# Kernel optimization log

Measured on AMD Instinct MI355X. Metric: run time of the kernel, lower is better.

The kernel has to match this reference:

```python
import jax, jax.numpy as jnp
import numpy as np
import math

DIM = 256
N = 4096
E = 1024
NEG = -1.0e9


def setup_inputs() -> dict:
    key = jax.random.key(0)
    ks = jax.random.split(key, 10)
    x = jax.random.normal(ks[0], (N, DIM), dtype=jnp.float32)
    # sparse incidence / adjacency (module only uses >0 as mask)
    H = (jax.random.uniform(ks[1], (N, E)) < 0.05).astype(jnp.float32)
    adj = (jax.random.uniform(ks[2], (N, N)) < 0.01).astype(jnp.float32)
    s = 1.0 / math.sqrt(DIM)
    W_he = jax.random.normal(ks[3], (DIM, DIM), dtype=jnp.float32) * s  # HyperedgeAttention.W
    u = jax.random.normal(ks[4], (DIM,), dtype=jnp.float32)            # HyperedgeAttention.u
    W_e = jax.random.normal(ks[5], (DIM, DIM), dtype=jnp.float32) * s  # NodeAttention.W_e
    W_n = jax.random.normal(ks[6], (DIM, DIM), dtype=jnp.float32) * s  # NodeAttention.W_n
    W_g = jax.random.normal(ks[7], (DIM, DIM), dtype=jnp.float32) * s  # GraphAttention.W
    a_g = jax.random.normal(ks[8], (2 * DIM,), dtype=jnp.float32) * s  # GraphAttention.attn weight
    return {"x": x, "H": H, "adj": adj, "W_he": W_he, "u": u,
            "W_e": W_e, "W_n": W_n, "W_g": W_g, "a_g": a_g}


def reference(x, H, adj, W_he, u, W_e, W_n, W_g, a_g):
    n, dim = x.shape
    inv_sqrt_d = 1.0 / math.sqrt(dim)
    maskH = H > 0                       # [N,E] bool
    mask_Hf = maskH.astype(x.dtype)

    # ---- HyperedgeAttention ----
    h_he = x @ W_he                     # [N,dim]
    sc = (h_he @ u) * inv_sqrt_d        # [N]
    scE = jnp.where(maskH, sc[:, None], NEG)      # [N,E]
    A = jax.nn.softmax(scE, axis=0) * mask_Hf     # column softmax over nodes
    e_repr = A.T @ h_he                 # [E,dim]

    # ---- NodeAttention (only B is used) ----
    hn = x @ W_n                        # [N,dim]
    he = e_repr @ W_e                   # [E,dim]
    Bsc = jnp.where(maskH, (hn @ he.T) * inv_sqrt_d, NEG)
    B = jax.nn.softmax(Bsc, axis=1) * mask_Hf     # [N,E]

    # ---- GraphAttention (concat score split: e_ij = lrelu(h_i.a1 + h_j.a2)) ----
    h_g = x @ W_g                       # [N,dim]
    s1 = h_g @ a_g[:dim]                # [N]
    s2 = h_g @ a_g[dim:]                # [N]
    e = jax.nn.leaky_relu(s1[:, None] + s2[None, :], 0.2)   # [N,N]
    maskA = (adj > 0).astype(x.dtype)
    sl = jnp.eye(n, dtype=x.dtype)
    e = e * (maskA + sl) - 1e9 * jnp.clip(1.0 - maskA - sl, 0.0, None)
    G = jax.nn.softmax(e, axis=1)       # [N,N]

    # ---- Mixing ----
    he_sz = jnp.clip(mask_Hf.sum(0), 1.0, None)   # [E]
    M = (G @ mask_Hf) / he_sz[None, :]            # [N,E]
    A_hat = jax.nn.softmax(A.T + M.T, axis=1) * mask_Hf.T   # [E,N]
    e_mix = A_hat @ (x @ W_he)                    # [E,dim]
    B_hat = jax.nn.softmax(B + M, axis=1) * mask_Hf          # [N,E]
    z_h = jax.nn.elu(B_hat @ (e_mix @ W_e))       # [N,dim]
    G_hat = jax.nn.softmax(G + B @ B.T + A @ A.T, axis=1)    # [N,N]
    z_g = jax.nn.elu(G_hat @ (x @ W_g))           # [N,dim]
    return z_h, z_g
```

## Files before the change

### kernel.cpp

```cpp
#include <hip/hip_runtime.h>
#include <math.h>
#include <stdint.h>

#define Nn 4096
#define Ee 1024
#define Dd 256

typedef __attribute__((ext_vector_type(8))) __bf16 bf16x8;
typedef __attribute__((ext_vector_type(4))) float f32x4;
typedef __attribute__((ext_vector_type(8))) unsigned short u16x8;

__device__ __forceinline__ unsigned short f2bf(float f) {
  unsigned int u = __float_as_uint(f);
  unsigned int r = (u + 0x7fffu + ((u >> 16) & 1u)) >> 16;
  return (unsigned short)r;
}

__device__ __forceinline__ void gload_lds16(const void* g, void* l) {
  __builtin_amdgcn_global_load_lds(
      (__attribute__((address_space(1))) void*)const_cast<void*>(g),
      (__attribute__((address_space(3))) void*)l, 16, 0, 0);
}

__device__ __forceinline__ float block_reduce_sum(float v) {
  __shared__ float sh[4];
  #pragma unroll
  for (int o = 32; o > 0; o >>= 1) v += __shfl_down(v, o);
  int lane = threadIdx.x & 63, w = threadIdx.x >> 6;
  if (lane == 0) sh[w] = v;
  __syncthreads();
  float s = sh[0] + sh[1] + sh[2] + sh[3];
  __syncthreads();
  return s;
}

__global__ __launch_bounds__(256) void gemm_bt_bf16(
    const unsigned short* __restrict__ Ab, const unsigned short* __restrict__ Bb,
    float* __restrict__ Cp, int M, int N, int K, const float* __restrict__ coldiv)
{
  __shared__ unsigned short As[2][128 * 32];
  __shared__ unsigned short Bs[2][128 * 32];
  const int tid = threadIdx.x;
  const int m0 = blockIdx.x * 128, n0 = blockIdx.y * 128;
  const int wave = tid >> 6, lane = tid & 63;
  const int wr = (wave >> 1) * 64, wc = (wave & 1) * 64;
  const int l16 = lane & 15, lq = lane >> 4;
  f32x4 acc[4][4] = {};
  const int NT = K >> 5;

  auto stage = [&](int buf, int kt) {
    const int k0 = kt * 32;
    #pragma unroll
    for (int i = 0; i < 2; ++i) {
      int t2 = tid + i * 256;
      int r = t2 >> 2, c = (t2 & 3) * 8;
      gload_lds16(Ab + (size_t)(m0 + r) * K + k0 + c, &As[buf][t2 * 8]);
    }
    #pragma unroll
    for (int i = 0; i < 2; ++i) {
      int t2 = tid + i * 256;
      int r = t2 >> 2, c = (t2 & 3) * 8;
      gload_lds16(Bb + (size_t)(n0 + r) * K + k0 + c, &Bs[buf][t2 * 8]);
    }
  };

  stage(0, 0);
  __syncthreads();
  int buf = 0;
  for (int kt = 0; kt < NT; ++kt) {
    if (kt + 1 < NT) stage(buf ^ 1, kt + 1);
    bf16x8 af[4], bfr[4];
    #pragma unroll
    for (int m = 0; m < 4; ++m)
      af[m] = *reinterpret_cast<const bf16x8*>(&As[buf][(wr + m * 16 + l16) * 32 + lq * 8]);
    #pragma unroll
    for (int n = 0; n < 4; ++n)
      bfr[n] = *reinterpret_cast<const bf16x8*>(&Bs[buf][(wc + n * 16 + l16) * 32 + lq * 8]);
    #pragma unroll
    for (int m = 0; m < 4; ++m)
      #pragma unroll
      for (int n = 0; n < 4; ++n)
        acc[m][n] = __builtin_amdgcn_mfma_f32_16x16x32_bf16(af[m], bfr[n], acc[m][n], 0, 0, 0);
    __syncthreads();
    buf ^= 1;
  }
  #pragma unroll
  for (int m = 0; m < 4; ++m)
    #pragma unroll
    for (int n = 0; n < 4; ++n) {
      int col = n0 + wc + n * 16 + l16;
      float cd = coldiv ? fmaxf(coldiv[col], 1.f) : 1.f;
      #pragma unroll
      for (int q = 0; q < 4; ++q) {
        int row = m0 + wr + m * 16 + lq * 4 + q;
        Cp[(size_t)row * N + col] = acc[m][n][q] / cd;
      }
    }
}

__global__ __launch_bounds__(256) void gemm_gram_k(
    const unsigned short* __restrict__ CAT,
    float* __restrict__ G,
    float* __restrict__ rowsum)
{
  const int K = 2048, N = Nn;
  __shared__ unsigned short As[2][128 * 32];
  __shared__ unsigned short Bs[2][128 * 32];
  const int tid = threadIdx.x;
  const int m0 = blockIdx.x * 128, n0 = blockIdx.y * 128;
  const int wave = tid >> 6, lane = tid & 63;
  const int wr = (wave >> 1) * 64, wc = (wave & 1) * 64;
  const int l16 = lane & 15, lq = lane >> 4;
  f32x4 acc[4][4] = {};
  const int NT = K >> 5;

  auto stage = [&](int buf, int kt) {
    const int k0 = kt * 32;
    #pragma unroll
    for (int i = 0; i < 2; ++i) {
      int t2 = tid + i * 256;
      int r = t2 >> 2, c = (t2 & 3) * 8;
      gload_lds16(CAT + (size_t)(m0 + r) * K + k0 + c, &As[buf][t2 * 8]);
    }
    #pragma unroll
    for (int i = 0; i < 2; ++i) {
      int t2 = tid + i * 256;
      int r = t2 >> 2, c = (t2 & 3) * 8;
      gload_lds16(CAT + (size_t)(n0 + r) * K + k0 + c, &Bs[buf][t2 * 8]);
    }
  };

  stage(0, 0);
  __syncthreads();
  int buf = 0;
  for (int kt = 0; kt < NT; ++kt) {
    if (kt + 1 < NT) stage(buf ^ 1, kt + 1);
    bf16x8 af[4], bfr[4];
    #pragma unroll
    for (int m = 0; m < 4; ++m)
      af[m] = *reinterpret_cast<const bf16x8*>(&As[buf][(wr + m * 16 + l16) * 32 + lq * 8]);
    #pragma unroll
    for (int n = 0; n < 4; ++n)
      bfr[n] = *reinterpret_cast<const bf16x8*>(&Bs[buf][(wc + n * 16 + l16) * 32 + lq * 8]);
    #pragma unroll
    for (int m = 0; m < 4; ++m)
      #pragma unroll
      for (int n = 0; n < 4; ++n)
        acc[m][n] = __builtin_amdgcn_mfma_f32_16x16x32_bf16(af[m], bfr[n], acc[m][n], 0, 0, 0);
    __syncthreads();
    buf ^= 1;
  }
  #pragma unroll
  for (int m = 0; m < 4; ++m)
    #pragma unroll
    for (int q = 0; q < 4; ++q) {
      int row = m0 + wr + m * 16 + lq * 4 + q;
      float s = 0.f;
      #pragma unroll
      for (int n = 0; n < 4; ++n) {
        int col = n0 + wc + n * 16 + l16;
        size_t idx = (size_t)row * N + col;
        float e = expf(G[idx] + acc[m][n][q]);
        G[idx] = e;
        s += e;
      }
      s += __shfl_xor(s, 1); s += __shfl_xor(s, 2);
      s += __shfl_xor(s, 4); s += __shfl_xor(s, 8);
      if (l16 == 0) atomicAdd(&rowsum[row], s);
    }
}

__global__ __launch_bounds__(256) void gemm64s_bt_bf16(
    const unsigned short* __restrict__ Ab, const unsigned short* __restrict__ Bb,
    float* __restrict__ Cp, int M, int N, int K, int KS)
{
  __shared__ unsigned short As[2][64 * 64];
  __shared__ unsigned short Bs[2][64 * 64];
  const int tid = threadIdx.x;
  const int m0 = blockIdx.x * 64, n0 = blockIdx.y * 64;
  const int kbase = blockIdx.z * KS;
  const int wave = tid >> 6, lane = tid & 63;
  const int wr = (wave >> 1) * 32, wc = (wave & 1) * 32;
  const int l16 = lane & 15, lq = lane >> 4;
  f32x4 acc[2][2] = {};
  const int NT = KS >> 6;

  auto stage = [&](int buf, int kt) {
    const int k0 = kbase + kt * 64;
    #pragma unroll
    for (int i = 0; i < 2; ++i) {
      int t2 = tid + i * 256;
      int r = t2 >> 3, c = (t2 & 7) * 8;
      gload_lds16(Ab + (size_t)(m0 + r) * K + k0 + c, &As[buf][t2 * 8]);
    }
    #pragma unroll
    for (int i = 0; i < 2; ++i) {
      int t2 = tid + i * 256;
      int r = t2 >> 3, c = (t2 & 7) * 8;
      gload_lds16(Bb + (size_t)(n0 + r) * K + k0 + c, &Bs[buf][t2 * 8]);
    }
  };

  stage(0, 0);
  __syncthreads();
  int buf = 0;
  for (int kt = 0; kt < NT; ++kt) {
    if (kt + 1 < NT) stage(buf ^ 1, kt + 1);
    bf16x8 af[2][2], bfr[2][2];
    #pragma unroll
    for (int m = 0; m < 2; ++m)
      #pragma unroll
      for (int ks = 0; ks < 2; ++ks)
        af[m][ks] = *reinterpret_cast<const bf16x8*>(
            &As[buf][(wr + m * 16 + l16) * 64 + ks * 32 + lq * 8]);
    #pragma unroll
    for (int n = 0; n < 2; ++n)
      #pragma unroll
      for (int ks = 0; ks < 2; ++ks)
        bfr[n][ks] = *reinterpret_cast<const bf16x8*>(
            &Bs[buf][(wc + n * 16 + l16) * 64 + ks * 32 + lq * 8]);
    #pragma unroll
    for (int m = 0; m < 2; ++m)
      #pragma unroll
      for (int n = 0; n < 2; ++n)
        #pragma unroll
        for (int ks = 0; ks < 2; ++ks)
          acc[m][n] = __builtin_amdgcn_mfma_f32_16x16x32_bf16(af[m][ks], bfr[n][ks], acc[m][n], 0, 0, 0);
    __syncthreads();
    buf ^= 1;
  }
  #pragma unroll
  for (int m = 0; m < 2; ++m)
    #pragma unroll
    for (int n = 0; n < 2; ++n) {
      int col = n0 + wc + n * 16 + l16;
      #pragma unroll
      for (int q = 0; q < 4; ++q) {
        int row = m0 + wr + m * 16 + lq * 4 + q;
        atomicAdd(&Cp[(size_t)row * N + col], acc[m][n][q]);
      }
    }
}

__global__ __launch_bounds__(256) void tcvt_k(const float* __restrict__ in,
                                              unsigned short* __restrict__ outT, int R, int S) {
  __shared__ unsigned short tile[64][65];
  int r0 = blockIdx.x * 64, c0 = blockIdx.y * 64;
  int t = threadIdx.x & 63, q = threadIdx.x >> 6;
  for (int rr = q; rr < 64; rr += 4)
    tile[t][rr] = f2bf(in[(long)(r0 + rr) * S + c0 + t]);
  __syncthreads();
  for (int cc = q; cc < 64; cc += 4)
    outT[(long)(c0 + cc) * R + r0 + t] = tile[cc][t];
}

__global__ __launch_bounds__(256) void elu_k(float* __restrict__ p, long n) {
  long i = ((long)blockIdx.x * 256 + threadIdx.x) * 4;
  if (i + 4 > n) return;
  float4 v = *reinterpret_cast<const float4*>(&p[i]);
  v.x = v.x > 0.f ? v.x : expm1f(v.x);
  v.y = v.y > 0.f ? v.y : expm1f(v.y);
  v.z = v.z > 0.f ? v.z : expm1f(v.z);
  v.w = v.w > 0.f ? v.w : expm1f(v.w);
  *reinterpret_cast<float4*>(&p[i]) = v;
}

__global__ __launch_bounds__(256) void wcat_k(const float* __restrict__ W0,
                                              const float* __restrict__ W1,
                                              const float* __restrict__ W2,
                                              float* __restrict__ Wcat) {
  int k = blockIdx.x, s = blockIdx.y, t = threadIdx.x;
  const float* W = s == 0 ? W0 : (s == 1 ? W1 : W2);
  Wcat[(long)k * 768 + s * 256 + t] = W[(long)k * 256 + t];
}

__global__ __launch_bounds__(256) void gemm64_k(
    const float* __restrict__ Ap, const float* __restrict__ Bp, float* __restrict__ Cp,
    int M, int N, int K, int Asm, int Ask, int Bsk, int Bsn)
{
  __shared__ alignas(16) float As[16][68];
  __shared__ alignas(16) float Bs[16][68];
  const int tid = threadIdx.x;
  const int tx = tid & 15, ty = tid >> 4;
  const int m0 = blockIdx.x * 64, n0 = blockIdx.y * 64;
  float acc[4][4] = {};
  for (int k0 = 0; k0 < K; k0 += 16) {
    if (Ask == 1) {
      int mm = tid >> 2, kk = (tid & 3) << 2;
      float4 v = *reinterpret_cast<const float4*>(&Ap[(long)(m0 + mm) * Asm + k0 + kk]);
      As[kk + 0][mm] = v.x; As[kk + 1][mm] = v.y; As[kk + 2][mm] = v.z; As[kk + 3][mm] = v.w;
    } else {
      int kk = tid >> 4, mm = (tid & 15) << 2;
      *reinterpret_cast<float4*>(&As[kk][mm]) =
          *reinterpret_cast<const float4*>(&Ap[(long)(k0 + kk) * Ask + m0 + mm]);
    }
    if (Bsn == 1) {
      int kk = tid >> 4, nn = (tid & 15) << 2;
      *reinterpret_cast<float4*>(&Bs[kk][nn]) =
          *reinterpret_cast<const float4*>(&Bp[(long)(k0 + kk) * Bsk + n0 + nn]);
    } else {
      int nn = tid >> 2, kk = (tid & 3) << 2;
      float4 v = *reinterpret_cast<const float4*>(&Bp[(long)(n0 + nn) * Bsn + k0 + kk]);
      Bs[kk + 0][nn] = v.x; Bs[kk + 1][nn] = v.y; Bs[kk + 2][nn] = v.z; Bs[kk + 3][nn] = v.w;
    }
    __syncthreads();
    #pragma unroll
    for (int kk = 0; kk < 16; ++kk) {
      float4 av = *reinterpret_cast<const float4*>(&As[kk][ty << 2]);
      float4 bv = *reinterpret_cast<const float4*>(&Bs[kk][tx << 2]);
      float a[4] = {av.x, av.y, av.z, av.w};
      float b[4] = {bv.x, bv.y, bv.z, bv.w};
      #pragma unroll
      for (int r = 0; r < 4; ++r)
        #pragma unroll
        for (int c = 0; c < 4; ++c) acc[r][c] = fmaf(a[r], b[c], acc[r][c]);
    }
    __syncthreads();
  }
  #pragma unroll
  for (int r = 0; r < 4; ++r) {
    long base = (long)(m0 + (ty << 2) + r) * N + n0 + (tx << 2);
    float4 o = {acc[r][0], acc[r][1], acc[r][2], acc[r][3]};
    *reinterpret_cast<float4*>(&Cp[base]) = o;
  }
}

__global__ __launch_bounds__(256) void gemm128_k(
    const float* __restrict__ Ap, const float* __restrict__ Bp, float* __restrict__ Cp,
    int M, int N, int K, int Asm, int Bsn, float alpha)
{
  __shared__ alignas(16) float As[16][132];
  __shared__ alignas(16) float Bs[16][132];
  const int tid = threadIdx.x;
  const int tx = tid & 15, ty = tid >> 4;
  const int m0 = blockIdx.x * 128, n0 = blockIdx.y * 128;
  float acc[2][2][4][4] = {};
  for (int k0 = 0; k0 < K; k0 += 16) {
    {
      int mm = tid >> 2, kk = (tid & 3) << 2;
      #pragma unroll
      for (int h = 0; h < 2; ++h) {
        float4 v = *reinterpret_cast<const float4*>(&Ap[(long)(m0 + mm + 64 * h) * Asm + k0 + kk]);
        As[kk + 0][mm + 64 * h] = v.x; As[kk + 1][mm + 64 * h] = v.y;
        As[kk + 2][mm + 64 * h] = v.z; As[kk + 3][mm + 64 * h] = v.w;
      }
    }
    {
      int nn = tid >> 2, kk = (tid & 3) << 2;
      #pragma unroll
      for (int h = 0; h < 2; ++h) {
        float4 v = *reinterpret_cast<const float4*>(&Bp[(long)(n0 + nn + 64 * h) * Bsn + k0 + kk]);
        Bs[kk + 0][nn + 64 * h] = v.x; Bs[kk + 1][nn + 64 * h] = v.y;
        Bs[kk + 2][nn + 64 * h] = v.z; Bs[kk + 3][nn + 64 * h] = v.w;
      }
    }
    __syncthreads();
    #pragma unroll
    for (int kk = 0; kk < 16; ++kk) {
      float a[2][4], b[2][4];
      #pragma unroll
      for (int h = 0; h < 2; ++h) {
        float4 av = *reinterpret_cast<const float4*>(&As[kk][(ty << 2) + 64 * h]);
        a[h][0] = av.x; a[h][1] = av.y; a[h][2] = av.z; a[h][3] = av.w;
        float4 bv = *reinterpret_cast<const float4*>(&Bs[kk][(tx << 2) + 64 * h]);
        b[h][0] = bv.x; b[h][1] = bv.y; b[h][2] = bv.z; b[h][3] = bv.w;
      }
      #pragma unroll
      for (int i = 0; i < 2; ++i)
        #pragma unroll
        for (int j = 0; j < 2; ++j)
          #pragma unroll
          for (int r = 0; r < 4; ++r)
            #pragma unroll
            for (int c = 0; c < 4; ++c)
              acc[i][j][r][c] = fmaf(a[i][r], b[j][c], acc[i][j][r][c]);
    }
    __syncthreads();
  }
  #pragma unroll
  for (int i = 0; i < 2; ++i)
    #pragma unroll
    for (int r = 0; r < 4; ++r) {
      int row = m0 + 64 * i + (ty << 2) + r;
      #pragma unroll
      for (int j = 0; j < 2; ++j) {
        long base = (long)row * N + n0 + 64 * j + (tx << 2);
        float4 o = {acc[i][j][r][0] * alpha, acc[i][j][r][1] * alpha,
                    acc[i][j][r][2] * alpha, acc[i][j][r][3] * alpha};
        *reinterpret_cast<float4*>(&Cp[base]) = o;
      }
    }
}

__global__ __launch_bounds__(256) void rowdots_k(
    const float* __restrict__ hcat, const float* __restrict__ u, const float* __restrict__ a_g,
    float* __restrict__ esc, float* __restrict__ s1, float* __restrict__ s2)
{
  int i = blockIdx.x, t = threadIdx.x;
  float hh = hcat[(long)i * 768 + t];
  float hg = hcat[(long)i * 768 + 512 + t];
  float d0 = block_reduce_sum(hh * u[t]);
  float d1 = block_reduce_sum(hg * a_g[t]);
  float d2 = block_reduce_sum(hg * a_g[Dd + t]);
  if (t == 0) {
    esc[i] = expf(d0 * 0.0625f);
    s1[i] = d1;
    s2[i] = d2;
  }
}

__global__ __launch_bounds__(256) void colstats_k(
    const float* __restrict__ H, const float* __restrict__ esc,
    float* __restrict__ colden, float* __restrict__ cnt)
{
  int e = blockIdx.x * 256 + threadIdx.x;
  int r0 = blockIdx.y * 128;
  float d = 0.f, c = 0.f;
  for (int r = r0; r < r0 + 128; ++r) {
    float h = H[(long)r * Ee + e];
    if (h > 0.f) { d += esc[r]; c += 1.f; }
  }
  atomicAdd(&colden[e], d);
  atomicAdd(&cnt[e], c);
}

__global__ __launch_bounds__(256) void fillA_k(
    const float* __restrict__ H, const float* __restrict__ esc,
    const float* __restrict__ colden, float* __restrict__ A,
    unsigned short* __restrict__ CAT)
{
  long base = ((long)blockIdx.x * 256 + threadIdx.x) * 4;
  int r = (int)(base >> 10);
  int e = (int)(base & 1023);
  float4 h = *reinterpret_cast<const float4*>(&H[base]);
  float4 cd = *reinterpret_cast<const float4*>(&colden[e]);
  float er = esc[r];
  float4 o;
  o.x = h.x > 0.f ? er / cd.x : 0.f;
  o.y = h.y > 0.f ? er / cd.y : 0.f;
  o.z = h.z > 0.f ? er / cd.z : 0.f;
  o.w = h.w > 0.f ? er / cd.w : 0.f;
  *reinterpret_cast<float4*>(&A[base]) = o;
  ushort4 ob = {f2bf(o.x), f2bf(o.y), f2bf(o.z), f2bf(o.w)};
  *reinterpret_cast<ushort4*>(&CAT[(long)r * 2048 + 1024 + e]) = ob;
}

__global__ __launch_bounds__(256) void brow_k(float* __restrict__ Bbuf,
                                              const float* __restrict__ H,
                                              unsigned short* __restrict__ CAT)
{
  int i = blockIdx.x, t = threadIdx.x;
  long base = (long)i * Ee + t * 4;
  float4 raw = *reinterpret_cast<const float4*>(&Bbuf[base]);
  float4 h = *reinterpret_cast<const float4*>(&H[base]);
  float rr[4] = {raw.x, raw.y, raw.z, raw.w}, hh[4] = {h.x, h.y, h.z, h.w};
  float p[4]; float s = 0.f;
  #pragma unroll
  for (int k = 0; k < 4; ++k) { p[k] = hh[k] > 0.f ? expf(rr[k]) : 0.f; s += p[k]; }
  float den = block_reduce_sum(s);
  float inv = den > 0.f ? 1.f / den : 0.f;
  float4 o = {p[0] * inv, p[1] * inv, p[2] * inv, p[3] * inv};
  *reinterpret_cast<float4*>(&Bbuf[base]) = o;
  ushort4 ob = {f2bf(o.x), f2bf(o.y), f2bf(o.z), f2bf(o.w)};
  *reinterpret_cast<ushort4*>(&CAT[(long)i * 2048 + t * 4]) = ob;
}

__global__ __launch_bounds__(256) void gfill_k(
    const float* __restrict__ adj, const float* __restrict__ s1,
    const float* __restrict__ s2, float* __restrict__ G, unsigned short* __restrict__ Gb)
{
  int i = blockIdx.x, t = threadIdx.x;
  float s1i = s1[i];
  float p[16]; float sum = 0.f;
  #pragma unroll
  for (int c = 0; c < 4; ++c) {
    int j = c * 1024 + t * 4;
    float4 a = *reinterpret_cast<const float4*>(&adj[(long)i * Nn + j]);
    float4 sv = *reinterpret_cast<const float4*>(&s2[j]);
    float aa[4] = {a.x, a.y, a.z, a.w}, ss[4] = {sv.x, sv.y, sv.z, sv.w};
    #pragma unroll
    for (int k = 0; k < 4; ++k) {
      float f = (aa[k] > 0.f ? 1.f : 0.f) + ((j + k) == i ? 1.f : 0.f);
      float l = s1i + ss[k];
      l = l > 0.f ? l : 0.2f * l;
      float val = l * f - 1e9f * fmaxf(1.f - f, 0.f);
      float pp = expf(val);
      p[c * 4 + k] = pp; sum += pp;
    }
  }
  float den = block_reduce_sum(sum);
  float inv = 1.f / den;
  #pragma unroll
  for (int c = 0; c < 4; ++c) {
    int j = c * 1024 + t * 4;
    float4 o = {p[c * 4] * inv, p[c * 4 + 1] * inv, p[c * 4 + 2] * inv, p[c * 4 + 3] * inv};
    *reinterpret_cast<float4*>(&G[(long)i * Nn + j]) = o;
    ushort4 ob = {f2bf(o.x), f2bf(o.y), f2bf(o.z), f2bf(o.w)};
    *reinterpret_cast<ushort4*>(&Gb[(long)i * Nn + j]) = ob;
  }
}

__global__ __launch_bounds__(256) void gscale_k(const float* __restrict__ expG,
                                                const float* __restrict__ rowsum,
                                                unsigned short* __restrict__ Gb)
{
  long i = ((long)blockIdx.x * 256 + threadIdx.x) * 8;
  int row = (int)(i >> 12);
  float inv = 1.f / rowsum[row];
  float4 a = *reinterpret_cast<const float4*>(&expG[i]);
  float4 b = *reinterpret_cast<const float4*>(&expG[i + 4]);
  u16x8 o;
  o[0] = f2bf(a.x * inv); o[1] = f2bf(a.y * inv); o[2] = f2bf(a.z * inv); o[3] = f2bf(a.w * inv);
  o[4] = f2bf(b.x * inv); o[5] = f2bf(b.y * inv); o[6] = f2bf(b.z * inv); o[7] = f2bf(b.w * inv);
  *reinterpret_cast<u16x8*>(&Gb[i]) = o;
}

__global__ __launch_bounds__(256) void amstats_k(
    const float* __restrict__ A, const float* __restrict__ Mm, float* __restrict__ aden)
{
  int e = blockIdx.x * 256 + threadIdx.x;
  int r0 = blockIdx.y * 128;
  float d = 0.f;
  for (int r = r0; r < r0 + 128; ++r) {
    long idx = (long)r * Ee + e;
    d += expf(A[idx] + Mm[idx]);
  }
  atomicAdd(&aden[e], d);
}

__global__ __launch_bounds__(256) void ahat_k(
    const float* __restrict__ Abuf, const float* __restrict__ Mm,
    const float* __restrict__ H, const float* __restrict__ aden,
    unsigned short* __restrict__ AhB)
{
  __shared__ float tile[64][65];
  int j0 = blockIdx.x * 64, e0 = blockIdx.y * 64;
  int te = threadIdx.x & 63;
  int tq = threadIdx.x >> 6;
  int e = e0 + te;
  float inv = 1.f / aden[e];
  for (int jj = tq; jj < 64; jj += 4) {
    long idx = (long)(j0 + jj) * Ee + e;
    float val = (H[idx] > 0.f) ? expf(Abuf[idx] + Mm[idx]) * inv : 0.f;
    tile[te][jj] = val;
  }
  __syncthreads();
  for (int ee = tq; ee < 64; ee += 4)
    AhB[(long)(e0 + ee) * Nn + j0 + te] = f2bf(tile[ee][te]);
}

__global__ __launch_bounds__(256) void bhat_k(const float* __restrict__ Bbuf,
                                              const float* __restrict__ Mm,
                                              const float* __restrict__ H,
                                              unsigned short* __restrict__ Bb2)
{
  int i = blockIdx.x, t = threadIdx.x;
  long base = (long)i * Ee + t * 4;
  float4 b = *reinterpret_cast<const float4*>(&Bbuf[base]);
  float4 m = *reinterpret_cast<const float4*>(&Mm[base]);
  float4 h = *reinterpret_cast<const float4*>(&H[base]);
  float bb[4] = {b.x, b.y, b.z, b.w}, mm2[4] = {m.x, m.y, m.z, m.w}, hh[4] = {h.x, h.y, h.z, h.w};
  float p[4]; float s = 0.f;
  #pragma unroll
  for (int k = 0; k < 4; ++k) { p[k] = expf(bb[k] + mm2[k]); s += p[k]; }
  float den = block_reduce_sum(s);
  float inv = 1.f / den;
  #pragma unroll
  for (int k = 0; k < 4; ++k) p[k] = hh[k] > 0.f ? p[k] * inv : 0.f;
  ushort4 ob = {f2bf(p[0]), f2bf(p[1]), f2bf(p[2]), f2bf(p[3])};
  *reinterpret_cast<ushort4*>(&Bb2[base]) = ob;
}

extern "C" void kernel_launch(void* const* d_in, const int* in_sizes, int n_in,
                              void* d_out, int out_size, void* d_ws, size_t ws_size,
                              hipStream_t stream) {
  const float* x    = (const float*)d_in[0];
  const float* H    = (const float*)d_in[1];
  const float* adj  = (const float*)d_in[2];
  const float* W_he = (const float*)d_in[3];
  const float* u    = (const float*)d_in[4];
  const float* W_e  = (const float*)d_in[5];
  const float* W_n  = (const float*)d_in[6];
  const float* W_g  = (const float*)d_in[7];
  const float* a_g  = (const float*)d_in[8];
  float* out = (float*)d_out;
  float* ws  = (float*)d_ws;
  (void)in_sizes; (void)n_in; (void)out_size; (void)ws_size;

  size_t off = 0;
  auto alloc = [&](size_t n) { float* p = ws + off; off += n; return p; };
  float* hcat   = alloc((size_t)Nn * 768);
  float* Wcat   = alloc((size_t)Dd * 768);
  float* esc    = alloc(Nn);
  float* s1     = alloc(Nn);
  float* s2     = alloc(Nn);
  float* colden = alloc(Ee);
  float* cnt    = alloc(Ee);
  float* aden   = alloc(Ee);
  float* rowsum = alloc(Nn);
  float* e_repr = alloc((size_t)Ee * Dd);
  float* e_mix  = alloc((size_t)Ee * Dd);
  float* heb    = alloc((size_t)Ee * Dd);
  float* tmp_ew = alloc((size_t)Ee * Dd);
  float* Abuf   = alloc((size_t)Nn * Ee);
  float* Bbuf   = alloc((size_t)Nn * Ee);
  float* Mm     = alloc((size_t)Nn * Ee);
  float* G      = alloc((size_t)Nn * Nn);
  unsigned short* Gb   = (unsigned short*)alloc((size_t)Nn * Nn / 2);
  unsigned short* CAT  = (unsigned short*)alloc((size_t)Nn * 2048 / 2);
  unsigned short* Hbt  = (unsigned short*)alloc((size_t)Ee * Nn / 2);
  unsigned short* AbT  = (unsigned short*)alloc((size_t)Ee * Nn / 2);
  unsigned short* AhB  = (unsigned short*)alloc((size_t)Ee * Nn / 2);
  unsigned short* hheT = (unsigned short*)alloc((size_t)Dd * Nn / 2);
  unsigned short* hgT  = (unsigned short*)alloc((size_t)Dd * Nn / 2);
  unsigned short* tewT = (unsigned short*)alloc((size_t)Dd * Ee / 2);
  unsigned short* Bb2  = (unsigned short*)alloc((size_t)Nn * Ee / 2);

  hipMemsetAsync(colden, 0, (3 * Ee + Nn) * sizeof(float), stream);
  hipMemsetAsync(e_repr, 0, 2 * (size_t)Ee * Dd * sizeof(float), stream);
  hipMemsetAsync(out, 0, 2 * (size_t)Nn * Dd * sizeof(float), stream);

  auto gs64 = [&](const unsigned short* A, const unsigned short* B, float* C,
                  int M, int N, int K, int KS) {
    gemm64s_bt_bf16<<<dim3(M / 64, N / 64, K / KS), 256, 0, stream>>>(A, B, C, M, N, K, KS);
  };
  auto tcvt = [&](const float* in, unsigned short* o, int R, int S, int cols) {
    tcvt_k<<<dim3(R / 64, cols / 64), 256, 0, stream>>>(in, o, R, S);
  };

  wcat_k<<<dim3(Dd, 3), 256, 0, stream>>>(W_he, W_n, W_g, Wcat);
  gemm64_k<<<dim3(Nn / 64, 768 / 64), 256, 0, stream>>>(x, Wcat, hcat, Nn, 768, Dd, Dd, 1, 768, 1);
  rowdots_k<<<Nn, 256, 0, stream>>>(hcat, u, a_g, esc, s1, s2);
  colstats_k<<<dim3(Ee / 256, 32), 256, 0, stream>>>(H, esc, colden, cnt);
  fillA_k<<<(Nn * Ee) / 1024, 256, 0, stream>>>(H, esc, colden, Abuf, CAT);
  tcvt(Abuf, AbT, Nn, Ee, Ee);
  tcvt(hcat, hheT, Nn, 768, Dd);
  gs64(AbT, hheT, e_repr, Ee, Dd, Nn, 1024);
  gemm64_k<<<dim3(Ee / 64, Dd / 64), 256, 0, stream>>>(e_repr, W_e, heb, Ee, Dd, Dd, Dd, 1, Dd, 1);
  gemm128_k<<<dim3(Nn / 128, Ee / 128), 256, 0, stream>>>(hcat + 256, heb, Bbuf, Nn, Ee, Dd, 768, Dd, 0.0625f);
  brow_k<<<Nn, 256, 0, stream>>>(Bbuf, H, CAT);
  gfill_k<<<Nn, 256, 0, stream>>>(adj, s1, s2, G, Gb);
  tcvt(H, Hbt, Nn, Ee, Ee);
  gemm_bt_bf16<<<dim3(Nn / 128, Ee / 128), 256, 0, stream>>>(Gb, Hbt, Mm, Nn, Ee, Nn, cnt);
  gemm_gram_k<<<dim3(Nn / 128, Nn / 128), 256, 0, stream>>>(CAT, G, rowsum);
  gscale_k<<<(int)(((size_t)Nn * Nn) / 2048), 256, 0, stream>>>(G, rowsum, Gb);
  amstats_k<<<dim3(Ee / 256, 32), 256, 0, stream>>>(Abuf, Mm, aden);
  ahat_k<<<dim3(Nn / 64, Ee / 64), 256, 0, stream>>>(Abuf, Mm, H, aden, AhB);
  gs64(AhB, hheT, e_mix, Ee, Dd, Nn, 1024);
  gemm64_k<<<dim3(Ee / 64, Dd / 64), 256, 0, stream>>>(e_mix, W_e, tmp_ew, Ee, Dd, Dd, Dd, 1, Dd, 1);
  bhat_k<<<Nn, 256, 0, stream>>>(Bbuf, Mm, H, Bb2);
  tcvt(tmp_ew, tewT, Ee, Dd, Dd);
  gs64(Bb2, tewT, out, Nn, Dd, Ee, Ee);
  tcvt(hcat + 512, hgT, Nn, 768, Dd);
  gs64(Gb, hgT, out + (size_t)Nn * Dd, Nn, Dd, Nn, 2048);
  elu_k<<<(2 * Nn * Dd) / 1024, 256, 0, stream>>>(out, 2L * Nn * Dd);
}
```

Measured before the change: 710.9 us.

## Use bf16 MFMA for projections, exploit Gram symmetry, defer softmax normalization

Result: faster. 665.4 us (-6.4%).

```diff
diff --git a/kernel.cpp b/kernel.cpp
--- a/kernel.cpp
+++ b/kernel.cpp
@@ -15,6 +15,9 @@
   unsigned int r = (u + 0x7fffu + ((u >> 16) & 1u)) >> 16;
   return (unsigned short)r;
 }
+__device__ __forceinline__ float bf2f(unsigned short u) {
+  return __uint_as_float(((unsigned int)u) << 16);
+}
 
 __device__ __forceinline__ void gload_lds16(const void* g, void* l) {
   __builtin_amdgcn_global_load_lds(
@@ -36,7 +39,9 @@
 
 __global__ __launch_bounds__(256) void gemm_bt_bf16(
     const unsigned short* __restrict__ Ab, const unsigned short* __restrict__ Bb,
-    float* __restrict__ Cp, int M, int N, int K, const float* __restrict__ coldiv)
+    float* __restrict__ Cp, unsigned short* __restrict__ Cb,
+    int M, int N, int K, int lda, int ldb, float alpha,
+    const float* __restrict__ coldiv)
 {
   __shared__ unsigned short As[2][128 * 32];
   __shared__ unsigned short Bs[2][128 * 32];
@@ -54,13 +59,13 @@
     for (int i = 0; i < 2; ++i) {
       int t2 = tid + i * 256;
       int r = t2 >> 2, c = (t2 & 3) * 8;
-      gload_lds16(Ab + (size_t)(m0 + r) * K + k0 + c, &As[buf][t2 * 8]);
+      gload_lds16(Ab + (size_t)(m0 + r) * lda + k0 + c, &As[buf][t2 * 8]);
     }
     #pragma unroll
     for (int i = 0; i < 2; ++i) {
       int t2 = tid + i * 256;
       int r = t2 >> 2, c = (t2 & 3) * 8;
-      gload_lds16(Bb + (size_t)(n0 + r) * K + k0 + c, &Bs[buf][t2 * 8]);
+      gload_lds16(Bb + (size_t)(n0 + r) * ldb + k0 + c, &Bs[buf][t2 * 8]);
     }
   };
 
@@ -93,21 +98,28 @@
       #pragma unroll
       for (int q = 0; q < 4; ++q) {
         int row = m0 + wr + m * 16 + lq * 4 + q;
-        Cp[(size_t)row * N + col] = acc[m][n][q] / cd;
+        size_t idx = (size_t)row * N + col;
+        float v = acc[m][n][q] * alpha / cd;
+        Cp[idx] = v;
+        if (Cb) Cb[idx] = f2bf(v);
       }
     }
 }
 
 __global__ __launch_bounds__(256) void gemm_gram_k(
     const unsigned short* __restrict__ CAT,
-    float* __restrict__ G,
+    const float* __restrict__ G,
+    unsigned short* __restrict__ Gb,
     float* __restrict__ rowsum)
 {
-  const int K = 2048, N = Nn;
-  __shared__ unsigned short As[2][128 * 32];
-  __shared__ unsigned short Bs[2][128 * 32];
+  const int bx = blockIdx.x, by = blockIdx.y;
+  if (bx > by) return;
+  const int K = 2048;
+  __shared__ unsigned short SM[17024];
+  unsigned short* Asb = SM;
+  unsigned short* Bsb = SM + 8192;
   const int tid = threadIdx.x;
-  const int m0 = blockIdx.x * 128, n0 = blockIdx.y * 128;
+  const int m0 = bx * 128, n0 = by * 128;
   const int wave = tid >> 6, lane = tid & 63;
   const int wr = (wave >> 1) * 64, wc = (wave & 1) * 64;
   const int l16 = lane & 15, lq = lane >> 4;
@@ -120,13 +132,13 @@
     for (int i = 0; i < 2; ++i) {
       int t2 = tid + i * 256;
       int r = t2 >> 2, c = (t2 & 3) * 8;
-      gload_lds16(CAT + (size_t)(m0 + r) * K + k0 + c, &As[buf][t2 * 8]);
+      gload_lds16(CAT + (size_t)(m0 + r) * K + k0 + c, Asb + buf * 4096 + t2 * 8);
     }
     #pragma unroll
     for (int i = 0; i < 2; ++i) {
       int t2 = tid + i * 256;
       int r = t2 >> 2, c = (t2 & 3) * 8;
-      gload_lds16(CAT + (size_t)(n0 + r) * K + k0 + c, &Bs[buf][t2 * 8]);
+      gload_lds16(CAT + (size_t)(n0 + r) * K + k0 + c, Bsb + buf * 4096 + t2 * 8);
     }
   };
 
@@ -138,10 +150,10 @@
     bf16x8 af[4], bfr[4];
     #pragma unroll
     for (int m = 0; m < 4; ++m)
-      af[m] = *reinterpret_cast<const bf16x8*>(&As[buf][(wr + m * 16 + l16) * 32 + lq * 8]);
+      af[m] = *reinterpret_cast<const bf16x8*>(Asb + buf * 4096 + (wr + m * 16 + l16) * 32 + lq * 8);
     #pragma unroll
     for (int n = 0; n < 4; ++n)
-      bfr[n] = *reinterpret_cast<const bf16x8*>(&Bs[buf][(wc + n * 16 + l16) * 32 + lq * 8]);
+      bfr[n] = *reinterpret_cast<const bf16x8*>(Bsb + buf * 4096 + (wc + n * 16 + l16) * 32 + lq * 8);
     #pragma unroll
     for (int m = 0; m < 4; ++m)
       #pragma unroll
@@ -159,15 +171,55 @@
       #pragma unroll
       for (int n = 0; n < 4; ++n) {
         int col = n0 + wc + n * 16 + l16;
-        size_t idx = (size_t)row * N + col;
+        size_t idx = (size_t)row * Nn + col;
         float e = expf(G[idx] + acc[m][n][q]);
-        G[idx] = e;
+        Gb[idx] = f2bf(e);
         s += e;
       }
       s += __shfl_xor(s, 1); s += __shfl_xor(s, 2);
       s += __shfl_xor(s, 4); s += __shfl_xor(s, 8);
       if (l16 == 0) atomicAdd(&rowsum[row], s);
     }
+  if (bx == by) return;
+
+  __syncthreads();
+  unsigned short* Tg = SM;
+  {
+    int cc = tid >> 1, r0 = (tid & 1) * 64;
+    const unsigned short* src = Gb + (size_t)(n0 + cc) * Nn + m0 + r0;
+    unsigned short* dst = Tg + cc * 132 + r0;
+    #pragma unroll
+    for (int v = 0; v < 8; ++v)
+      *reinterpret_cast<u16x8*>(dst + v * 8) = *reinterpret_cast<const u16x8*>(src + v * 8);
+  }
+  __syncthreads();
+  #pragma unroll
+  for (int n = 0; n < 4; ++n) {
+    int ccl = wc + n * 16 + l16;
+    float cs = 0.f;
+    #pragma unroll
+    for (int m = 0; m < 4; ++m) {
+      int sa = ccl * 132 + wr + m * 16 + lq * 4;
+      ushort4 lg = *reinterpret_cast<const ushort4*>(&Tg[sa]);
+      ushort4 eo;
+      float e0 = expf(bf2f(lg.x) + acc[m][n][0]); eo.x = f2bf(e0); cs += e0;
+      float e1 = expf(bf2f(lg.y) + acc[m][n][1]); eo.y = f2bf(e1); cs += e1;
+      float e2 = expf(bf2f(lg.z) + acc[m][n][2]); eo.z = f2bf(e2); cs += e2;
+      float e3 = expf(bf2f(lg.w) + acc[m][n][3]); eo.w = f2bf(e3); cs += e3;
+      *reinterpret_cast<ushort4*>(&Tg[sa]) = eo;
+    }
+    cs += __shfl_xor(cs, 16); cs += __shfl_xor(cs, 32);
+    if (lq == 0) atomicAdd(&rowsum[n0 + ccl], cs);
+  }
+  __syncthreads();
+  {
+    int cc = tid >> 1, r0 = (tid & 1) * 64;
+    const unsigned short* src = Tg + cc * 132 + r0;
+    unsigned short* dst = Gb + (size_t)(n0 + cc) * Nn + m0 + r0;
+    #pragma unroll
+    for (int v = 0; v < 8; ++v)
+      *reinterpret_cast<u16x8*>(dst + v * 8) = *reinterpret_cast<const u16x8*>(src + v * 8);
+  }
 }
 
 __global__ __launch_bounds__(256) void gemm64s_bt_bf16(
@@ -242,6 +294,18 @@
     }
 }
 
+__global__ __launch_bounds__(256) void cvt_bf16_k(const float* __restrict__ in,
+                                                  unsigned short* __restrict__ out, long n) {
+  long i = ((long)blockIdx.x * 256 + threadIdx.x) * 8;
+  if (i + 8 > n) return;
+  float4 a = *reinterpret_cast<const float4*>(&in[i]);
+  float4 b = *reinterpret_cast<const float4*>(&in[i + 4]);
+  u16x8 o;
+  o[0] = f2bf(a.x); o[1] = f2bf(a.y); o[2] = f2bf(a.z); o[3] = f2bf(a.w);
+  o[4] = f2bf(b.x); o[5] = f2bf(b.y); o[6] = f2bf(b.z); o[7] = f2bf(b.w);
+  *reinterpret_cast<u16x8*>(&out[i]) = o;
+}
+
 __global__ __launch_bounds__(256) void tcvt_k(const float* __restrict__ in,
                                               unsigned short* __restrict__ outT, int R, int S) {
   __shared__ unsigned short tile[64][65];
@@ -254,10 +318,14 @@
     outT[(long)(c0 + cc) * R + r0 + t] = tile[cc][t];
 }
 
-__global__ __launch_bounds__(256) void elu_k(float* __restrict__ p, long n) {
+__global__ __launch_bounds__(256) void elu_rows_k(float* __restrict__ p,
+                                                  const float* __restrict__ rowsum) {
   long i = ((long)blockIdx.x * 256 + threadIdx.x) * 4;
-  if (i + 4 > n) return;
   float4 v = *reinterpret_cast<const float4*>(&p[i]);
+  float sc = 1.f;
+  long half = (long)Nn * Dd;
+  if (i >= half) sc = 1.f / rowsum[(i - half) >> 8];
+  v.x *= sc; v.y *= sc; v.z *= sc; v.w *= sc;
   v.x = v.x > 0.f ? v.x : expm1f(v.x);
   v.y = v.y > 0.f ? v.y : expm1f(v.y);
   v.z = v.z > 0.f ? v.z : expm1f(v.z);
@@ -265,17 +333,9 @@
   *reinterpret_cast<float4*>(&p[i]) = v;
 }
 
-__global__ __launch_bounds__(256) void wcat_k(const float* __restrict__ W0,
-                                              const float* __restrict__ W1,
-                                              const float* __restrict__ W2,
-                                              float* __restrict__ Wcat) {
-  int k = blockIdx.x, s = blockIdx.y, t = threadIdx.x;
-  const float* W = s == 0 ? W0 : (s == 1 ? W1 : W2);
-  Wcat[(long)k * 768 + s * 256 + t] = W[(long)k * 256 + t];
-}
-
 __global__ __launch_bounds__(256) void gemm64_k(
     const float* __restrict__ Ap, const float* __restrict__ Bp, float* __restrict__ Cp,
+    unsigned short* __restrict__ Cb,
     int M, int N, int K, int Asm, int Ask, int Bsk, int Bsn)
 {
   __shared__ alignas(16) float As[16][68];
@@ -322,74 +382,11 @@
     long base = (long)(m0 + (ty << 2) + r) * N + n0 + (tx << 2);
     float4 o = {acc[r][0], acc[r][1], acc[r][2], acc[r][3]};
     *reinterpret_cast<float4*>(&Cp[base]) = o;
-  }
-}
-
-__global__ __launch_bounds__(256) void gemm128_k(
-    const float* __restrict__ Ap, const float* __restrict__ Bp, float* __restrict__ Cp,
-    int M, int N, int K, int Asm, int Bsn, float alpha)
-{
-  __shared__ alignas(16) float As[16][132];
-  __shared__ alignas(16) float Bs[16][132];
-  const int tid = threadIdx.x;
-  const int tx = tid & 15, ty = tid >> 4;
-  const int m0 = blockIdx.x * 128, n0 = blockIdx.y * 128;
-  float acc[2][2][4][4] = {};
-  for (int k0 = 0; k0 < K; k0 += 16) {
-    {
-      int mm = tid >> 2, kk = (tid & 3) << 2;
-      #pragma unroll
-      for (int h = 0; h < 2; ++h) {
-        float4 v = *reinterpret_cast<const float4*>(&Ap[(long)(m0 + mm + 64 * h) * Asm + k0 + kk]);
-        As[kk + 0][mm + 64 * h] = v.x; As[kk + 1][mm + 64 * h] = v.y;
-        As[kk + 2][mm + 64 * h] = v.z; As[kk + 3][mm + 64 * h] = v.w;
-      }
-    }
-    {
-      int nn = tid >> 2, kk = (tid & 3) << 2;
-      #pragma unroll
-      for (int h = 0; h < 2; ++h) {
-        float4 v = *reinterpret_cast<const float4*>(&Bp[(long)(n0 + nn + 64 * h) * Bsn + k0 + kk]);
-        Bs[kk + 0][nn + 64 * h] = v.x; Bs[kk + 1][nn + 64 * h] = v.y;
-        Bs[kk + 2][nn + 64 * h] = v.z; Bs[kk + 3][nn + 64 * h] = v.w;
-      }
-    }
-    __syncthreads();
-    #pragma unroll
-    for (int kk = 0; kk < 16; ++kk) {
-      float a[2][4], b[2][4];
-      #pragma unroll
-      for (int h = 0; h < 2; ++h) {
-        float4 av = *reinterpret_cast<const float4*>(&As[kk][(ty << 2) + 64 * h]);
-        a[h][0] = av.x; a[h][1] = av.y; a[h][2] = av.z; a[h][3] = av.w;
-        float4 bv = *reinterpret_cast<const float4*>(&Bs[kk][(tx << 2) + 64 * h]);
-        b[h][0] = bv.x; b[h][1] = bv.y; b[h][2] = bv.z; b[h][3] = bv.w;
-      }
-      #pragma unroll
-      for (int i = 0; i < 2; ++i)
-        #pragma unroll
-        for (int j = 0; j < 2; ++j)
-          #pragma unroll
-          for (int r = 0; r < 4; ++r)
-            #pragma unroll
-            for (int c = 0; c < 4; ++c)
-              acc[i][j][r][c] = fmaf(a[i][r], b[j][c], acc[i][j][r][c]);
-    }
-    __syncthreads();
-  }
-  #pragma unroll
-  for (int i = 0; i < 2; ++i)
-    #pragma unroll
-    for (int r = 0; r < 4; ++r) {
-      int row = m0 + 64 * i + (ty << 2) + r;
-      #pragma unroll
-      for (int j = 0; j < 2; ++j) {
-        long base = (long)row * N + n0 + 64 * j + (tx << 2);
-        float4 o = {acc[i][j][r][0] * alpha, acc[i][j][r][1] * alpha,
-                    acc[i][j][r][2] * alpha, acc[i][j][r][3] * alpha};
-        *reinterpret_cast<float4*>(&Cp[base]) = o;
-      }
-    }
+    if (Cb) {
+      ushort4 ob = {f2bf(o.x), f2bf(o.y), f2bf(o.z), f2bf(o.w)};
+      *reinterpret_cast<ushort4*>(&Cb[base]) = ob;
+    }
+  }
 }
 
 __global__ __launch_bounds__(256) void rowdots_k(
@@ -427,22 +424,24 @@
 __global__ __launch_bounds__(256) void fillA_k(
     const float* __restrict__ H, const float* __restrict__ esc,
     const float* __restrict__ colden, float* __restrict__ A,
-    unsigned short* __restrict__ CAT)
-{
-  long base = ((long)blockIdx.x * 256 + threadIdx.x) * 4;
-  int r = (int)(base >> 10);
-  int e = (int)(base & 1023);
-  float4 h = *reinterpret_cast<const float4*>(&H[base]);
-  float4 cd = *reinterpret_cast<const float4*>(&colden[e]);
-  float er = esc[r];
-  float4 o;
-  o.x = h.x > 0.f ? er / cd.x : 0.f;
-  o.y = h.y > 0.f ? er / cd.y : 0.f;
-  o.z = h.z > 0.f ? er / cd.z : 0.f;
-  o.w = h.w > 0.f ? er / cd.w : 0.f;
-  *reinterpret_cast<float4*>(&A[base]) = o;
-  ushort4 ob = {f2bf(o.x), f2bf(o.y), f2bf(o.z), f2bf(o.w)};
-  *reinterpret_cast<ushort4*>(&CAT[(long)r * 2048 + 1024 + e]) = ob;
+    unsigned short* __restrict__ CAT, unsigned short* __restrict__ AbT)
+{
+  __shared__ unsigned short tile[64][68];
+  int r0 = blockIdx.x * 64, e0 = blockIdx.y * 64;
+  int te = threadIdx.x & 63, tq = threadIdx.x >> 6;
+  float cd = colden[e0 + te];
+  for (int rr = tq; rr < 64; rr += 4) {
+    long idx = (long)(r0 + rr) * Ee + e0 + te;
+    float h = H[idx];
+    float val = h > 0.f ? esc[r0 + rr] / cd : 0.f;
+    A[idx] = val;
+    unsigned short vb = f2bf(val);
+    CAT[(long)(r0 + rr) * 2048 + 1024 + e0 + te] = vb;
+    tile[te][rr] = vb;
+  }
+  __syncthreads();
+  for (int ee = tq; ee < 64; ee += 4)
+    AbT[(long)(e0 + ee) * Nn + r0 + te] = tile[ee][te];
 }
 
 __global__ __launch_bounds__(256) void brow_k(float* __restrict__ Bbuf,
@@ -498,21 +497,6 @@
     ushort4 ob = {f2bf(o.x), f2bf(o.y), f2bf(o.z), f2bf(o.w)};
     *reinterpret_cast<ushort4*>(&Gb[(long)i * Nn + j]) = ob;
   }
-}
-
-__global__ __launch_bounds__(256) void gscale_k(const float* __restrict__ expG,
-                                                const float* __restrict__ rowsum,
-                                                unsigned short* __restrict__ Gb)
-{
-  long i = ((long)blockIdx.x * 256 + threadIdx.x) * 8;
-  int row = (int)(i >> 12);
-  float inv = 1.f / rowsum[row];
-  float4 a = *reinterpret_cast<const float4*>(&expG[i]);
-  float4 b = *reinterpret_cast<const float4*>(&expG[i + 4]);
-  u16x8 o;
-  o[0] = f2bf(a.x * inv); o[1] = f2bf(a.y * inv); o[2] = f2bf(a.z * inv); o[3] = f2bf(a.w * inv);
-  o[4] = f2bf(b.x * inv); o[5] = f2bf(b.y * inv); o[6] = f2bf(b.z * inv); o[7] = f2bf(b.w * inv);
-  *reinterpret_cast<u16x8*>(&Gb[i]) = o;
 }
 
 __global__ __launch_bounds__(256) void amstats_k(
@@ -590,7 +574,6 @@
   size_t off = 0;
   auto alloc = [&](size_t n) { float* p = ws + off; off += n; return p; };
   float* hcat   = alloc((size_t)Nn * 768);
-  float* Wcat   = alloc((size_t)Dd * 768);
   float* esc    = alloc(Nn);
   float* s1     = alloc(Nn);
   float* s2     = alloc(Nn);
@@ -606,20 +589,29 @@
   float* Bbuf   = alloc((size_t)Nn * Ee);
   float* Mm     = alloc((size_t)Nn * Ee);
   float* G      = alloc((size_t)Nn * Nn);
-  unsigned short* Gb   = (unsigned short*)alloc((size_t)Nn * Nn / 2);
-  unsigned short* CAT  = (unsigned short*)alloc((size_t)Nn * 2048 / 2);
-  unsigned short* Hbt  = (unsigned short*)alloc((size_t)Ee * Nn / 2);
-  unsigned short* AbT  = (unsigned short*)alloc((size_t)Ee * Nn / 2);
-  unsigned short* AhB  = (unsigned short*)alloc((size_t)Ee * Nn / 2);
-  unsigned short* hheT = (unsigned short*)alloc((size_t)Dd * Nn / 2);
-  unsigned short* hgT  = (unsigned short*)alloc((size_t)Dd * Nn / 2);
-  unsigned short* tewT = (unsigned short*)alloc((size_t)Dd * Ee / 2);
-  unsigned short* Bb2  = (unsigned short*)alloc((size_t)Nn * Ee / 2);
+  unsigned short* Gb    = (unsigned short*)alloc((size_t)Nn * Nn / 2);
+  unsigned short* CAT   = (unsigned short*)alloc((size_t)Nn * 2048 / 2);
+  unsigned short* Hbt   = (unsigned short*)alloc((size_t)Ee * Nn / 2);
+  unsigned short* AbT   = (unsigned short*)alloc((size_t)Ee * Nn / 2);
+  unsigned short* AhB   = (unsigned short*)alloc((size_t)Ee * Nn / 2);
+  unsigned short* hheT  = (unsigned short*)alloc((size_t)Dd * Nn / 2);
+  unsigned short* hgT   = (unsigned short*)alloc((size_t)Dd * Nn / 2);
+  unsigned short* tewT  = (unsigned short*)alloc((size_t)Dd * Ee / 2);
+  unsigned short* Bb2   = (unsigned short*)alloc((size_t)Nn * Ee / 2);
+  unsigned short* xb    = (unsigned short*)alloc((size_t)Nn * Dd / 2);
+  unsigned short* WcTb  = (unsigned short*)alloc((size_t)768 * Dd / 2);
+  unsigned short* hcatB = (unsigned short*)alloc((size_t)Nn * 768 / 2);
+  unsigned short* hebB  = (unsigned short*)alloc((size_t)Ee * Dd / 2);
 
   hipMemsetAsync(colden, 0, (3 * Ee + Nn) * sizeof(float), stream);
   hipMemsetAsync(e_repr, 0, 2 * (size_t)Ee * Dd * sizeof(float), stream);
   hipMemsetAsync(out, 0, 2 * (size_t)Nn * Dd * sizeof(float), stream);
 
+  auto gbt = [&](const unsigned short* A, const unsigned short* B, float* C, unsigned short* Cb,
+                 int M, int N, int K, int lda, int ldb, float alpha, const float* cd) {
+    gemm_bt_bf16<<<dim3(M / 128, N / 128), 256, 0, stream>>>(A, B, C, Cb, M, N, K, lda, ldb,
+                                                             alpha, cd);
+  };
   auto gs64 = [&](const unsigned short* A, const unsigned short* B, float* C,
                   int M, int N, int K, int KS) {
     gemm64s_bt_bf16<<<dim3(M / 64, N / 64, K / KS), 256, 0, stream>>>(A, B, C, M, N, K, KS);
@@ -628,30 +620,31 @@
     tcvt_k<<<dim3(R / 64, cols / 64), 256, 0, stream>>>(in, o, R, S);
   };
 
-  wcat_k<<<dim3(Dd, 3), 256, 0, stream>>>(W_he, W_n, W_g, Wcat);
-  gemm64_k<<<dim3(Nn / 64, 768 / 64), 256, 0, stream>>>(x, Wcat, hcat, Nn, 768, Dd, Dd, 1, 768, 1);
+  cvt_bf16_k<<<(Nn * Dd) / 2048, 256, 0, stream>>>(x, xb, (long)Nn * Dd);
+  tcvt(W_he, WcTb, Dd, Dd, Dd);
+  tcvt(W_n, WcTb + 256 * 256, Dd, Dd, Dd);
+  tcvt(W_g, WcTb + 2 * 256 * 256, Dd, Dd, Dd);
+  gbt(xb, WcTb, hcat, hcatB, Nn, 768, Dd, Dd, Dd, 1.f, nullptr);
   rowdots_k<<<Nn, 256, 0, stream>>>(hcat, u, a_g, esc, s1, s2);
   colstats_k<<<dim3(Ee / 256, 32), 256, 0, stream>>>(H, esc, colden, cnt);
-  fillA_k<<<(Nn * Ee) / 1024, 256, 0, stream>>>(H, esc, colden, Abuf, CAT);
-  tcvt(Abuf, AbT, Nn, Ee, Ee);
+  fillA_k<<<dim3(Nn / 64, Ee / 64), 256, 0, stream>>>(H, esc, colden, Abuf, CAT, AbT);
   tcvt(hcat, hheT, Nn, 768, Dd);
   gs64(AbT, hheT, e_repr, Ee, Dd, Nn, 1024);
-  gemm64_k<<<dim3(Ee / 64, Dd / 64), 256, 0, stream>>>(e_repr, W_e, heb, Ee, Dd, Dd, Dd, 1, Dd, 1);
-  gemm128_k<<<dim3(Nn / 128, Ee / 128), 256, 0, stream>>>(hcat + 256, heb, Bbuf, Nn, Ee, Dd, 768, Dd, 0.0625f);
+  gemm64_k<<<dim3(Ee / 64, Dd / 64), 256, 0, stream>>>(e_repr, W_e, heb, hebB, Ee, Dd, Dd, Dd, 1, Dd, 1);
+  gbt(hcatB + 256, hebB, Bbuf, nullptr, Nn, Ee, Dd, 768, Dd, 0.0625f, nullptr);
   brow_k<<<Nn, 256, 0, stream>>>(Bbuf, H, CAT);
   gfill_k<<<Nn, 256, 0, stream>>>(adj, s1, s2, G, Gb);
   tcvt(H, Hbt, Nn, Ee, Ee);
-  gemm_bt_bf16<<<dim3(Nn / 128, Ee / 128), 256, 0, stream>>>(Gb, Hbt, Mm, Nn, Ee, Nn, cnt);
-  gemm_gram_k<<<dim3(Nn / 128, Nn / 128), 256, 0, stream>>>(CAT, G, rowsum);
-  gscale_k<<<(int)(((size_t)Nn * Nn) / 2048), 256, 0, stream>>>(G, rowsum, Gb);
+  gbt(Gb, Hbt, Mm, nullptr, Nn, Ee, Nn, Nn, Nn, 1.f, cnt);
+  gemm_gram_k<<<dim3(Nn / 128, Nn / 128), 256, 0, stream>>>(CAT, G, Gb, rowsum);
   amstats_k<<<dim3(Ee / 256, 32), 256, 0, stream>>>(Abuf, Mm, aden);
   ahat_k<<<dim3(Nn / 64, Ee / 64), 256, 0, stream>>>(Abuf, Mm, H, aden, AhB);
   gs64(AhB, hheT, e_mix, Ee, Dd, Nn, 1024);
-  gemm64_k<<<dim3(Ee / 64, Dd / 64), 256, 0, stream>>>(e_mix, W_e, tmp_ew, Ee, Dd, Dd, Dd, 1, Dd, 1);
+  gemm64_k<<<dim3(Ee / 64, Dd / 64), 256, 0, stream>>>(e_mix, W_e, tmp_ew, nullptr, Ee, Dd, Dd, Dd, 1, Dd, 1);
   bhat_k<<<Nn, 256, 0, stream>>>(Bbuf, Mm, H, Bb2);
   tcvt(tmp_ew, tewT, Ee, Dd, Dd);
-  gs64(Bb2, tewT, out, Nn, Dd, Ee, Ee);
+  gs64(Bb2, tewT, out, Nn, Dd, Ee, 1024);
   tcvt(hcat + 512, hgT, Nn, 768, Dd);
   gs64(Gb, hgT, out + (size_t)Nn * Dd, Nn, Dd, Nn, 2048);
-  elu_k<<<(2 * Nn * Dd) / 1024, 256, 0, stream>>>(out, 2L * Nn * Dd);
-}
+  elu_rows_k<<<(2 * Nn * Dd) / 1024, 256, 0, stream>>>(out, rowsum);
+}
```
